# Optimization experiments

Hardware: AMD Instinct MI355X
Metric: run time of the kernel (lower is better)

The kernel has to match this reference:

```python
import jax, jax.numpy as jnp
import numpy as np

N = 32768      # total nodes
G = 64         # graphs
NPG = 512      # nodes per graph (equal-size graphs)
K = 256        # ceil(NPG * pooling_ratio), pooling_ratio=0.5
D = 256        # input_dim
H = 256        # hidden_dim
FD = 3 * H     # fusion dim
C = 10         # num_classes
E = 262144     # edges
EPS = 1e-5     # BatchNorm eps


def setup_inputs() -> dict:
    key = jax.random.key(0)
    ks = jax.random.split(key, 20)
    w = lambda k, s: jax.random.normal(k, s, jnp.float32) * 0.05
    inp = {
        'x': jax.random.normal(ks[0], (N, D), jnp.float32),
        'edge_index': jax.random.randint(ks[1], (2, E), 0, N, jnp.int64),
        'batch': (jnp.arange(N, dtype=jnp.int64) // NPG),
        'w_s1': w(ks[2], (D, H)), 'b_s1': jnp.zeros((H,), jnp.float32),
        'w_s21': w(ks[3], (D, H)), 'b_s21': jnp.zeros((H,), jnp.float32),
        'w_s22': w(ks[4], (H, H)), 'b_s22': jnp.zeros((H,), jnp.float32),
        'w_raw': w(ks[5], (D, H)), 'b_raw': jnp.zeros((H,), jnp.float32),
        'w_pos': w(ks[6], (FD, 1)), 'b_pos': jnp.zeros((1,), jnp.float32),
        'w_neg': w(ks[7], (FD, 1)), 'b_neg': jnp.zeros((1,), jnp.float32),
        'w_pool': w(ks[8], (FD, FD)), 'b_pool': jnp.zeros((FD,), jnp.float32),
        'w1': w(ks[9], (2 * FD, 256)), 'b1': jnp.zeros((256,), jnp.float32),
        'g1': jnp.ones((256,), jnp.float32), 'be1': jnp.zeros((256,), jnp.float32),
        'w2': w(ks[10], (256, 256)), 'b2': jnp.zeros((256,), jnp.float32),
        'g2': jnp.ones((256,), jnp.float32), 'be2': jnp.zeros((256,), jnp.float32),
        'w3': w(ks[11], (256, 256)), 'b3': jnp.zeros((256,), jnp.float32),
        'g3': jnp.ones((256,), jnp.float32), 'be3': jnp.zeros((256,), jnp.float32),
        'w4': w(ks[12], (256, C)), 'b4': jnp.zeros((C,), jnp.float32),
    }
    return inp


def _gcn(x, W, b, src, dst, dinv):
    # PyG GCNConv: linear, then sym-normalized aggregation with self-loops
    h = x @ W
    norm = dinv[src] * dinv[dst]
    agg = jax.ops.segment_sum(h[src] * norm[:, None], dst, num_segments=N)
    agg = agg + h * (dinv * dinv)[:, None]  # self-loop contribution
    return agg + b


def _bn(z, g, b):
    m = z.mean(0)
    v = z.var(0)  # biased, as torch BN training-mode normalization
    return (z - m) * jax.lax.rsqrt(v + EPS) * g + b


def _mlp(z, w1, b1, g1, be1, w2, b2, g2, be2, w3, b3, g3, be3, w4, b4):
    z = jax.nn.relu(_bn(z @ w1 + b1, g1, be1))  # dropout=identity (eval)
    idt = z
    o = jax.nn.relu(_bn(z @ w2 + b2, g2, be2))
    z = o + idt
    idt = z
    o = jax.nn.relu(_bn(z @ w3 + b3, g3, be3))
    z = o + idt
    return z @ w4 + b4


def _topk_mask(scores):
    # equal-size graphs -> per-graph top-k via one batched lax.top_k
    sg = scores.reshape(G, NPG)
    _, idx = jax.lax.top_k(sg, K)
    mask = jnp.zeros((G, NPG), bool).at[jnp.arange(G)[:, None], idx].set(True)
    return mask.reshape(-1)


def _readout(xt, mask):
    m = mask[:, None]
    xs = jnp.where(m, xt, 0.0).reshape(G, NPG, FD)
    mean_pool = xs.sum(1) / K
    mx = jnp.where(m, xt, -jnp.inf).reshape(G, NPG, FD).max(1)
    return jnp.concatenate([mean_pool, mx], axis=1)


def reference(x, edge_index, batch, w_s1, b_s1, w_s21, b_s21, w_s22, b_s22,
              w_raw, b_raw, w_pos, b_pos, w_neg, b_neg, w_pool, b_pool,
              w1, b1, g1, be1, w2, b2, g2, be2, w3, b3, g3, be3, w4, b4):
    src, dst = edge_index[0], edge_index[1]
    deg = jax.ops.segment_sum(jnp.ones_like(src, jnp.float32), dst, num_segments=N) + 1.0
    dinv = jax.lax.rsqrt(deg)
    lrelu = lambda z: jax.nn.leaky_relu(z, 0.01)

    h_s1 = lrelu(_gcn(x, w_s1, b_s1, src, dst, dinv))
    h_s2 = lrelu(_gcn(lrelu(_gcn(x, w_s21, b_s21, src, dst, dinv)), w_s22, b_s22, src, dst, dinv))
    h_raw = x @ w_raw + b_raw
    h_final = jnp.concatenate([h_s1, h_s2, h_raw], axis=1)  # [N, FD]

    score_pos = jax.nn.sigmoid(_gcn(h_final, w_pos, b_pos, src, dst, dinv)).reshape(-1)
    score_neg = jax.nn.sigmoid(_gcn(h_final, w_neg, b_neg, src, dst, dinv)).reshape(-1)

    xt = jax.nn.sigmoid(h_final @ w_pool + b_pool)  # pool_transform for all nodes; mask selects
    mask_pos = _topk_mask(score_pos)
    mask_neg = _topk_mask(score_neg)

    mlp = lambda e: _mlp(e, w1, b1, g1, be1, w2, b2, g2, be2, w3, b3, g3, be3, w4, b4)
    logits_pos = mlp(_readout(xt, mask_pos))
    probs_pos = jax.nn.softmax(logits_pos, axis=1)
    logits_neg = mlp(_readout(xt, mask_neg))
    probs_neg = jax.nn.softmax(logits_neg, axis=1)
    return (logits_pos, probs_pos, probs_neg, score_pos, score_neg, batch)
```

## Files before the change

### kernel.cpp

```cpp
#include <hip/hip_runtime.h>
#include <hip/hip_bf16.h>

#define N_NODES 32768
#define NGRAPH  64
#define NPG     512
#define TOPK    256
#define HID     256
#define FDIM    768
#define NEDGE   262144
#define NCLS    10
#define BN_EPS  1e-5f

#define IN_BF16 0
#define OUT_BF16 0

typedef __attribute__((ext_vector_type(8))) short short8;
typedef __attribute__((ext_vector_type(4))) float f32x4;

__device__ __forceinline__ float bf2f(unsigned short u) {
    return __uint_as_float(((unsigned)u) << 16);
}
__device__ __forceinline__ unsigned short f2bf(float f) {
    unsigned x = __float_as_uint(f);
    unsigned r = (x + 0x7fffu + ((x >> 16) & 1u)) >> 16;
    return (unsigned short)r;
}
__device__ __forceinline__ float in_ld(const void* p, size_t i) {
#if IN_BF16
    return bf2f(((const unsigned short*)p)[i]);
#else
    return ((const float*)p)[i];
#endif
}
__device__ __forceinline__ void st_out(void* o, size_t i, float v) {
#if OUT_BF16
    ((unsigned short*)o)[i] = f2bf(v);
#else
    ((float*)o)[i] = v;
#endif
}

__device__ __forceinline__ void async_cp16(const unsigned short* g, unsigned short* l) {
    __builtin_amdgcn_global_load_lds(
        (const __attribute__((address_space(1))) unsigned int*)g,
        (__attribute__((address_space(3))) unsigned int*)l, 16, 0, 0);
}

__device__ __forceinline__ void tile_swizzle(int& bm, int& bn) {
    int nx = gridDim.x;
    int L = blockIdx.y * nx + blockIdx.x;
    int xcd = L & 7;
    int j = L >> 3;
    bm = ((j / nx) * 8 + xcd) * 128;
    bn = (j % nx) * 128;
}

__global__ __launch_bounds__(256) void cvt_kernel(const float* __restrict__ in,
                                                  unsigned short* __restrict__ out, int n) {
    int i = blockIdx.x * 256 + threadIdx.x;
    if (i < n) out[i] = f2bf(in[i]);
}

__global__ __launch_bounds__(256) void cvt_t_all_kernel(const float* __restrict__ w_s1,
                                                        const float* __restrict__ w_s21,
                                                        const float* __restrict__ w_raw,
                                                        const float* __restrict__ w_s22,
                                                        const float* __restrict__ w_pool,
                                                        unsigned short* __restrict__ wcat,
                                                        unsigned short* __restrict__ wb_s22,
                                                        unsigned short* __restrict__ wb_pool) {
    __shared__ unsigned short tile[32][33];
    int id = blockIdx.x;
    const float* src;
    unsigned short* dst;
    int K, N, t;
    if (id < 64)       { src = w_s1;  dst = wcat;                       K = 256; N = 256; t = id; }
    else if (id < 128) { src = w_s21; dst = wcat + (size_t)256 * 256;   K = 256; N = 256; t = id - 64; }
    else if (id < 192) { src = w_raw; dst = wcat + (size_t)512 * 256;   K = 256; N = 256; t = id - 128; }
    else if (id < 256) { src = w_s22; dst = wb_s22;                     K = 256; N = 256; t = id - 192; }
    else               { src = w_pool; dst = wb_pool;                   K = 768; N = 768; t = id - 256; }
    int tiles_x = K >> 5;
    int bk = (t % tiles_x) * 32, bn = (t / tiles_x) * 32;
    int tx = threadIdx.x & 31, ty = threadIdx.x >> 5;
#pragma unroll
    for (int i = 0; i < 32; i += 8)
        tile[ty + i][tx] = f2bf(src[(size_t)(bk + ty + i) * N + bn + tx]);
    __syncthreads();
#pragma unroll
    for (int i = 0; i < 32; i += 8)
        dst[(size_t)(bn + ty + i) * K + bk + tx] = tile[tx][ty + i];
}

__global__ __launch_bounds__(256) void detect_kernel(const int* __restrict__ eb, int* __restrict__ flag) {
    int i = blockIdx.x * 256 + threadIdx.x;
    int v = eb[2 * (size_t)i + 1];
    unsigned long long b = __ballot(v != 0);
    if ((threadIdx.x & 63) == 0 && b)
        atomicAdd(flag, (int)__popcll(b));
}

__global__ __launch_bounds__(256) void hist_kernel(const int* __restrict__ eb, const int* __restrict__ flag,
                                                   int* __restrict__ deg) {
    int e = blockIdx.x * 256 + threadIdx.x;
    int st = (*flag == 0) ? 2 : 1;
    unsigned d = ((const unsigned*)eb)[(size_t)(NEDGE + e) * st] & (N_NODES - 1);
    atomicAdd(&deg[d], 1);
}

__global__ __launch_bounds__(1024) void scan_kernel(const int* __restrict__ cnt, int* __restrict__ rowptr,
                                                    int* __restrict__ cursor, float* __restrict__ dinv) {
    __shared__ int part[1024];
    int t = threadIdx.x;
    int base = t * 32;
    int loc[32];
    int s = 0;
#pragma unroll
    for (int i = 0; i < 32; i++) { loc[i] = cnt[base + i]; s += loc[i]; }
    part[t] = s;
    __syncthreads();
    for (int off = 1; off < 1024; off <<= 1) {
        int v = (t >= off) ? part[t - off] : 0;
        __syncthreads();
        part[t] += v;
        __syncthreads();
    }
    int run = (t == 0) ? 0 : part[t - 1];
#pragma unroll
    for (int i = 0; i < 32; i++) {
        rowptr[base + i] = run;
        cursor[base + i] = run;
        dinv[base + i] = rsqrtf((float)loc[i] + 1.0f);
        run += loc[i];
    }
    if (t == 1023) rowptr[N_NODES] = run;
}

__global__ __launch_bounds__(256) void scatter_kernel(const int* __restrict__ eb, const int* __restrict__ flag,
                                                      int* __restrict__ cursor, int* __restrict__ srcs) {
    int e = blockIdx.x * 256 + threadIdx.x;
    int st = (*flag == 0) ? 2 : 1;
    unsigned s = ((const unsigned*)eb)[(size_t)e * st] & (N_NODES - 1);
    unsigned d = ((const unsigned*)eb)[(size_t)(NEDGE + e) * st] & (N_NODES - 1);
    int p = atomicAdd(&cursor[d], 1);
    srcs[p] = (int)s;
}

#define GEMM_CORE(K_)                                                           \
    __shared__ unsigned short As[128 * 64];                                     \
    __shared__ unsigned short Bs[128 * 64];                                     \
    const int tid = threadIdx.x;                                                \
    const int wave = tid >> 6;                                                  \
    const int lane = tid & 63;                                                  \
    int bm, bn;                                                                 \
    tile_swizzle(bm, bn);                                                       \
    const int wm = (wave >> 1) * 64;                                            \
    const int wn = (wave & 1) * 64;                                             \
    const int l15 = lane & 15;                                                  \
    const int q = lane >> 4;                                                    \
    f32x4 acc[4][4] = {};                                                       \
    const int srow = lane >> 3;                                                 \
    const int schunk = lane & 7;                                                \
    const int gc = schunk ^ srow;                                               \
    const unsigned short* gaA = A + (size_t)(bm + wave * 8 + srow) * (K_) + gc * 8;  \
    const unsigned short* gbB = WT + (size_t)(bn + wave * 8 + srow) * (K_) + gc * 8; \
    const size_t K32 = (size_t)(K_) * 32;                                       \
    unsigned short* const la0 = &As[(wave * 8) * 64];                           \
    unsigned short* const lb0 = &Bs[(wave * 8) * 64];                           \
    for (int k0 = 0; k0 < (K_); k0 += 64) {                                     \
        __syncthreads();                                                        \
        _Pragma("unroll")                                                       \
        for (int t = 0; t < 4; t++) {                                           \
            async_cp16(gaA + t * K32 + k0, la0 + t * 32 * 64);                  \
            async_cp16(gbB + t * K32 + k0, lb0 + t * 32 * 64);                  \
        }                                                                       \
        __syncthreads();                                                        \
        _Pragma("unroll")                                                       \
        for (int h = 0; h < 2; h++) {                                           \
            short8 af[4], bfv[4];                                               \
            int p = (h * 4 + q) ^ (l15 & 7);                                    \
            _Pragma("unroll")                                                   \
            for (int t = 0; t < 4; t++) {                                       \
                int m = wm + t * 16 + l15;                                      \
                int n = wn + t * 16 + l15;                                      \
                af[t] = *(const short8*)&As[m * 64 + p * 8];                    \
                bfv[t] = *(const short8*)&Bs[n * 64 + p * 8];                   \
            }                                                                   \
            _Pragma("unroll")                                                   \
            for (int tm = 0; tm < 4; tm++)                                      \
                _Pragma("unroll")                                               \
                for (int tn = 0; tn < 4; tn++)                                  \
                    acc[tm][tn] = __builtin_amdgcn_mfma_f32_16x16x32_bf16(af[tm], bfv[tn], acc[tm][tn], 0, 0, 0); \
        }                                                                       \
    }

__global__ __launch_bounds__(256) void gemm_kernel(const unsigned short* __restrict__ A,
                                                   const unsigned short* __restrict__ WT,
                                                   const float* __restrict__ bias,
                                                   unsigned short* __restrict__ C,
                                                   int K, int ldC, int colOff, int epi) {
    GEMM_CORE(K)
#pragma unroll
    for (int tm = 0; tm < 4; tm++) {
        int row = bm + wm + tm * 16 + q * 4;
#pragma unroll
        for (int tn = 0; tn < 4; tn++) {
            int col = bn + wn + tn * 16 + l15;
            float bv = bias ? bias[col] : 0.0f;
#pragma unroll
            for (int r = 0; r < 4; r++) {
                float v = acc[tm][tn][r] + bv;
                if (epi == 1) v = 1.0f / (1.0f + __expf(-v));
                C[(size_t)(row + r) * ldC + colOff + col] = f2bf(v);
            }
        }
    }
}

__global__ __launch_bounds__(256) void gemm3_kernel(const unsigned short* __restrict__ A,
                                                    const unsigned short* __restrict__ WT,
                                                    const float* __restrict__ b_raw,
                                                    unsigned short* __restrict__ tA,
                                                    unsigned short* __restrict__ tB,
                                                    unsigned short* __restrict__ hfin) {
    GEMM_CORE(256)
#pragma unroll
    for (int tm = 0; tm < 4; tm++) {
        int row = bm + wm + tm * 16 + q * 4;
#pragma unroll
        for (int tn = 0; tn < 4; tn++) {
            int col = bn + wn + tn * 16 + l15;
            if (col < 256) {
#pragma unroll
                for (int r = 0; r < 4; r++)
                    tA[(size_t)(row + r) * 256 + col] = f2bf(acc[tm][tn][r]);
            } else if (col < 512) {
#pragma unroll
                for (int r = 0; r < 4; r++)
                    tB[(size_t)(row + r) * 256 + (col - 256)] = f2bf(acc[tm][tn][r]);
            } else {
                float bv = b_raw[col - 512];
#pragma unroll
                for (int r = 0; r < 4; r++)
                    hfin[(size_t)(row + r) * 768 + col] = f2bf(acc[tm][tn][r] + bv);
            }
        }
    }
}

__global__ __launch_bounds__(256) void agg2_kernel(const unsigned short* __restrict__ hA,
                                                   const unsigned short* __restrict__ hB,
                                                   const int* __restrict__ rowptr, const int* __restrict__ srcs,
                                                   const float* __restrict__ dinv,
                                                   const float* __restrict__ biasA, const float* __restrict__ biasB,
                                                   unsigned short* __restrict__ outA,
                                                   unsigned short* __restrict__ outB) {
    int wave = threadIdx.x >> 6, lane = threadIdx.x & 63;
    int v = blockIdx.x * 4 + wave;
    int f0 = lane * 4;
    float a0 = 0.f, a1 = 0.f, a2 = 0.f, a3 = 0.f;
    float c0 = 0.f, c1 = 0.f, c2 = 0.f, c3 = 0.f;
    int s = rowptr[v], e = rowptr[v + 1];
    for (int i = s; i < e; i++) {
        int u = srcs[i] & (N_NODES - 1);
        float du = dinv[u];
        uint2 ha = *(const uint2*)(hA + (size_t)u * 256 + f0);
        uint2 hb = *(const uint2*)(hB + (size_t)u * 256 + f0);
        a0 += bf2f((unsigned short)(ha.x & 0xffff)) * du;
        a1 += bf2f((unsigned short)(ha.x >> 16)) * du;
        a2 += bf2f((unsigned short)(ha.y & 0xffff)) * du;
        a3 += bf2f((unsigned short)(ha.y >> 16)) * du;
        c0 += bf2f((unsigned short)(hb.x & 0xffff)) * du;
        c1 += bf2f((unsigned short)(hb.x >> 16)) * du;
        c2 += bf2f((unsigned short)(hb.y & 0xffff)) * du;
        c3 += bf2f((unsigned short)(hb.y >> 16)) * du;
    }
    float dv = dinv[v], dv2 = dv * dv;
    uint2 sa = *(const uint2*)(hA + (size_t)v * 256 + f0);
    uint2 sb = *(const uint2*)(hB + (size_t)v * 256 + f0);
    float r0 = dv * a0 + bf2f((unsigned short)(sa.x & 0xffff)) * dv2 + biasA[f0 + 0];
    float r1 = dv * a1 + bf2f((unsigned short)(sa.x >> 16)) * dv2 + biasA[f0 + 1];
    float r2 = dv * a2 + bf2f((unsigned short)(sa.y & 0xffff)) * dv2 + biasA[f0 + 2];
    float r3 = dv * a3 + bf2f((unsigned short)(sa.y >> 16)) * dv2 + biasA[f0 + 3];
    float t0 = dv * c0 + bf2f((unsigned short)(sb.x & 0xffff)) * dv2 + biasB[f0 + 0];
    float t1 = dv * c1 + bf2f((unsigned short)(sb.x >> 16)) * dv2 + biasB[f0 + 1];
    float t2 = dv * c2 + bf2f((unsigned short)(sb.y & 0xffff)) * dv2 + biasB[f0 + 2];
    float t3 = dv * c3 + bf2f((unsigned short)(sb.y >> 16)) * dv2 + biasB[f0 + 3];
    r0 = r0 > 0.f ? r0 : 0.01f * r0;  r1 = r1 > 0.f ? r1 : 0.01f * r1;
    r2 = r2 > 0.f ? r2 : 0.01f * r2;  r3 = r3 > 0.f ? r3 : 0.01f * r3;
    t0 = t0 > 0.f ? t0 : 0.01f * t0;  t1 = t1 > 0.f ? t1 : 0.01f * t1;
    t2 = t2 > 0.f ? t2 : 0.01f * t2;  t3 = t3 > 0.f ? t3 : 0.01f * t3;
    uint2 ov = make_uint2(((unsigned)f2bf(r1) << 16) | f2bf(r0), ((unsigned)f2bf(r3) << 16) | f2bf(r2));
    uint2 ow = make_uint2(((unsigned)f2bf(t1) << 16) | f2bf(t0), ((unsigned)f2bf(t3) << 16) | f2bf(t2));
    *(uint2*)(outA + (size_t)v * 768 + f0) = ov;
    *(uint2*)(outB + (size_t)v * 256 + f0) = ow;
}

__global__ __launch_bounds__(256) void agg_kernel(const unsigned short* __restrict__ h,
                                                  const int* __restrict__ rowptr, const int* __restrict__ srcs,
                                                  const float* __restrict__ dinv, const float* __restrict__ bias,
                                                  unsigned short* __restrict__ out, int ldOut, int colOff,
                                                  int do_lrelu) {
    int wave = threadIdx.x >> 6, lane = threadIdx.x & 63;
    int v = blockIdx.x * 4 + wave;
    int f0 = lane * 4;
    float a0 = 0.f, a1 = 0.f, a2 = 0.f, a3 = 0.f;
    int s = rowptr[v], e = rowptr[v + 1];
    for (int i = s; i < e; i++) {
        int u = srcs[i] & (N_NODES - 1);
        float du = dinv[u];
        uint2 hv = *(const uint2*)(h + (size_t)u * 256 + f0);
        a0 += bf2f((unsigned short)(hv.x & 0xffff)) * du;
        a1 += bf2f((unsigned short)(hv.x >> 16)) * du;
        a2 += bf2f((unsigned short)(hv.y & 0xffff)) * du;
        a3 += bf2f((unsigned short)(hv.y >> 16)) * du;
    }
    float dv = dinv[v], dv2 = dv * dv;
    uint2 sv = *(const uint2*)(h + (size_t)v * 256 + f0);
    float r0 = dv * a0 + bf2f((unsigned short)(sv.x & 0xffff)) * dv2 + bias[f0 + 0];
    float r1 = dv * a1 + bf2f((unsigned short)(sv.x >> 16)) * dv2 + bias[f0 + 1];
    float r2 = dv * a2 + bf2f((unsigned short)(sv.y & 0xffff)) * dv2 + bias[f0 + 2];
    float r3 = dv * a3 + bf2f((unsigned short)(sv.y >> 16)) * dv2 + bias[f0 + 3];
    if (do_lrelu) {
        r0 = r0 > 0.f ? r0 : 0.01f * r0;
        r1 = r1 > 0.f ? r1 : 0.01f * r1;
        r2 = r2 > 0.f ? r2 : 0.01f * r2;
        r3 = r3 > 0.f ? r3 : 0.01f * r3;
    }
    uint2 ov = make_uint2(((unsigned)f2bf(r1) << 16) | f2bf(r0), ((unsigned)f2bf(r3) << 16) | f2bf(r2));
    *(uint2*)(out + (size_t)v * ldOut + colOff + f0) = ov;
}

__global__ __launch_bounds__(256) void score_mv_kernel(const unsigned short* __restrict__ hf,
                                                       const void* __restrict__ wp, const void* __restrict__ wn,
                                                       float* __restrict__ svp, float* __restrict__ svn) {
    int wave = threadIdx.x >> 6, lane = threadIdx.x & 63;
    int v = blockIdx.x * 4 + wave;
    float sp = 0.f, sn = 0.f;
#pragma unroll
    for (int i = 0; i < 3; i++) {
        int k = i * 256 + lane * 4;
        uint2 hv = *(const uint2*)(hf + (size_t)v * 768 + k);
        float x0 = bf2f((unsigned short)(hv.x & 0xffff));
        float x1 = bf2f((unsigned short)(hv.x >> 16));
        float x2 = bf2f((unsigned short)(hv.y & 0xffff));
        float x3 = bf2f((unsigned short)(hv.y >> 16));
        sp += x0 * in_ld(wp, k) + x1 * in_ld(wp, k + 1) + x2 * in_ld(wp, k + 2) + x3 * in_ld(wp, k + 3);
        sn += x0 * in_ld(wn, k) + x1 * in_ld(wn, k + 1) + x2 * in_ld(wn, k + 2) + x3 * in_ld(wn, k + 3);
    }
    for (int off = 32; off >= 1; off >>= 1) {
        sp += __shfl_down(sp, off, 64);
        sn += __shfl_down(sn, off, 64);
    }
    if (lane == 0) { svp[v] = sp; svn[v] = sn; }
}

__global__ __launch_bounds__(256) void score_agg_kernel(const float* __restrict__ svp, const float* __restrict__ svn,
                                                        const int* __restrict__ rowptr, const int* __restrict__ srcs,
                                                        const float* __restrict__ dinv,
                                                        const void* __restrict__ bp, const void* __restrict__ bn_,
                                                        float* __restrict__ scp, float* __restrict__ scn,
                                                        void* __restrict__ dout) {
    int v = blockIdx.x * 256 + threadIdx.x;
    float ap = 0.f, an = 0.f;
    int s = rowptr[v], e = rowptr[v + 1];
    for (int i = s; i < e; i++) {
        int u = srcs[i] & (N_NODES - 1);
        float du = dinv[u];
        ap += svp[u] * du;
        an += svn[u] * du;
    }
    float dv = dinv[v], dv2 = dv * dv;
    float zp = dv * ap + svp[v] * dv2 + in_ld(bp, 0);
    float zn = dv * an + svn[v] * dv2 + in_ld(bn_, 0);
    float pp = 1.0f / (1.0f + __expf(-zp));
    float pn = 1.0f / (1.0f + __expf(-zn));
    scp[v] = pp;
    scn[v] = pn;
    st_out(dout, 1920 + (size_t)v, pp);
    st_out(dout, 1920 + (size_t)N_NODES + v, pn);
    st_out(dout, 1920 + 2 * (size_t)N_NODES + v, (float)(v >> 9));
}

__global__ __launch_bounds__(512) void topk2_kernel(const float* __restrict__ scp, const float* __restrict__ scn,
                                                    unsigned char* __restrict__ maskp,
                                                    unsigned char* __restrict__ maskn) {
    __shared__ float s[512];
    const float* sc = (blockIdx.x & 1) ? scn : scp;
    unsigned char* mask = (blockIdx.x & 1) ? maskn : maskp;
    int g = blockIdx.x >> 1, i = threadIdx.x;
    float my = sc[(size_t)g * 512 + i];
    s[i] = my;
    __syncthreads();
    int cnt = 0;
    for (int j = 0; j < 512; j++) {
        float o = s[j];
        cnt += (int)((o > my) || ((o == my) && (j < i)));
    }
    mask[(size_t)g * 512 + i] = (cnt < TOPK) ? 1 : 0;
}

__global__ __launch_bounds__(256) void readout2_kernel(const unsigned short* __restrict__ xt,
                                                       const unsigned char* __restrict__ maskp,
                                                       const unsigned char* __restrict__ maskn,
                                                       float* __restrict__ eout) {
    int g = blockIdx.x;
    int c = blockIdx.y;
    int wv = threadIdx.x >> 6, lane = threadIdx.x & 63;
    int f = c * 64 + lane;
    __shared__ unsigned char mp[512], mn[512];
    __shared__ float red[4][64][4];
    for (int i = threadIdx.x; i < 512; i += 256) {
        mp[i] = maskp[(size_t)g * 512 + i];
        mn[i] = maskn[(size_t)g * 512 + i];
    }
    __syncthreads();
    float sp = 0.f, sn = 0.f, xp = -INFINITY, xn = -INFINITY;
    const unsigned short* base = xt + ((size_t)g * 512 + wv * 128) * 768 + f;
    for (int v = 0; v < 128; v++) {
        unsigned char bp = mp[wv * 128 + v], bn_ = mn[wv * 128 + v];
        if (!(bp | bn_)) continue;
        float x = bf2f(base[(size_t)v * 768]);
        if (bp) { sp += x; xp = fmaxf(xp, x); }
        if (bn_) { sn += x; xn = fmaxf(xn, x); }
    }
    red[wv][lane][0] = sp; red[wv][lane][1] = xp;
    red[wv][lane][2] = sn; red[wv][lane][3] = xn;
    __syncthreads();
    if (wv == 0) {
#pragma unroll
        for (int w = 1; w < 4; w++) {
            sp += red[w][lane][0]; xp = fmaxf(xp, red[w][lane][1]);
            sn += red[w][lane][2]; xn = fmaxf(xn, red[w][lane][3]);
        }
        float* erp = eout + (size_t)g * 1536;
        float* ern = eout + (size_t)(64 + g) * 1536;
        erp[f] = sp * (1.0f / TOPK);
        erp[768 + f] = xp;
        ern[f] = sn * (1.0f / TOPK);
        ern[768 + f] = xn;
    }
}

__global__ __launch_bounds__(256) void mlp_gemm2_kernel(const float* __restrict__ in,
                                                        const float* __restrict__ W,
                                                        const float* __restrict__ b,
                                                        float* __restrict__ out, int K) {
    __shared__ float row[1536];
    __shared__ float red[4][64];
    int r = blockIdx.x, cg = blockIdx.y;
    int wv = threadIdx.x >> 6, lane = threadIdx.x & 63;
    int c = cg * 64 + lane;
    for (int k = threadIdx.x; k < K; k += 256) row[k] = in[(size_t)r * K + k];
    __syncthreads();
    int kpw = K >> 2;
    const float* wp = W + (size_t)(wv * kpw) * 256 + c;
    const float* rp = row + wv * kpw;
    float acc = 0.f;
#pragma unroll 4
    for (int k = 0; k < kpw; k++)
        acc += rp[k] * wp[(size_t)k * 256];
    red[wv][lane] = acc;
    __syncthreads();
    if (wv == 0) {
        float v = red[0][lane] + red[1][lane] + red[2][lane] + red[3][lane] + b[c];
        out[(size_t)r * 256 + c] = v;
    }
}

__global__ __launch_bounds__(64) void bn_kernel(const float* __restrict__ z, const void* __restrict__ gamma,
                                                const void* __restrict__ beta, const float* __restrict__ res,
                                                float* __restrict__ out) {
    int f = blockIdx.x & 255, g = blockIdx.x >> 8, r = threadIdx.x;
    size_t idx = (size_t)(g * 64 + r) * 256 + f;
    float x = z[idx];
    float s = x, sq = x * x;
    for (int off = 1; off < 64; off <<= 1) {
        s += __shfl_xor(s, off, 64);
        sq += __shfl_xor(sq, off, 64);
    }
    float m = s * (1.0f / 64.0f);
    float var = sq * (1.0f / 64.0f) - m * m;
    float y = (x - m) * rsqrtf(var + BN_EPS) * in_ld(gamma, f) + in_ld(beta, f);
    y = fmaxf(y, 0.0f);
    if (res) y += res[idx];
    out[idx] = y;
}

__global__ __launch_bounds__(64) void logits_kernel(const float* __restrict__ act, const void* __restrict__ w4,
                                                    const void* __restrict__ b4, float* __restrict__ lg) {
    int idx = blockIdx.x * 64 + threadIdx.x;
    if (idx >= 128 * NCLS) return;
    int r = idx / NCLS, c = idx % NCLS;
    float acc = in_ld(b4, c);
    for (int k = 0; k < 256; k++) acc += act[(size_t)r * 256 + k] * in_ld(w4, (size_t)k * NCLS + c);
    lg[idx] = acc;
}

__global__ __launch_bounds__(64) void softmax_kernel(const float* __restrict__ lg, void* __restrict__ dout) {
    int r = blockIdx.x * 64 + threadIdx.x;
    if (r >= 128) return;
    float l[NCLS];
    float mx = -1e30f;
    for (int c = 0; c < NCLS; c++) { l[c] = lg[(size_t)r * NCLS + c]; mx = fmaxf(mx, l[c]); }
    float sum = 0.f;
    float ex[NCLS];
    for (int c = 0; c < NCLS; c++) { ex[c] = __expf(l[c] - mx); sum += ex[c]; }
    float inv = 1.0f / sum;
    int g = r >> 6, rr = r & 63;
    if (g == 0) {
        for (int c = 0; c < NCLS; c++) st_out(dout, (size_t)rr * NCLS + c, l[c]);
        for (int c = 0; c < NCLS; c++) st_out(dout, 640 + (size_t)rr * NCLS + c, ex[c] * inv);
    } else {
        for (int c = 0; c < NCLS; c++) st_out(dout, 1280 + (size_t)rr * NCLS + c, ex[c] * inv);
    }
}

extern "C" void kernel_launch(void* const* d_in, const int* in_sizes, int n_in,
                              void* d_out, int out_size, void* d_ws, size_t ws_size,
                              hipStream_t stream) {
    (void)in_sizes; (void)n_in; (void)out_size; (void)ws_size;

    const float* x = (const float*)d_in[0];
    const int* eb = (const int*)d_in[1];
    const float* w_s1 = (const float*)d_in[3];
    const float* b_s1 = (const float*)d_in[4];
    const float* w_s21 = (const float*)d_in[5];
    const float* b_s21 = (const float*)d_in[6];
    const float* w_s22 = (const float*)d_in[7];
    const float* b_s22 = (const float*)d_in[8];
    const float* w_raw = (const float*)d_in[9];
    const float* b_raw = (const float*)d_in[10];
    const void* w_pos = d_in[11];
    const void* b_pos = d_in[12];
    const void* w_neg = d_in[13];
    const void* b_neg = d_in[14];
    const float* w_pool = (const float*)d_in[15];
    const float* b_pool = (const float*)d_in[16];
    const float* w1 = (const float*)d_in[17];  const float* b1 = (const float*)d_in[18];
    const void* g1 = d_in[19];  const void* be1 = d_in[20];
    const float* w2 = (const float*)d_in[21];  const float* b2 = (const float*)d_in[22];
    const void* g2 = d_in[23];  const void* be2 = d_in[24];
    const float* w3 = (const float*)d_in[25];  const float* b3 = (const float*)d_in[26];
    const void* g3 = d_in[27];  const void* be3 = d_in[28];
    const void* w4 = d_in[29];  const void* b4 = d_in[30];

    char* ws = (char*)d_ws;
    size_t off = 0;
    auto alloc = [&](size_t b) -> void* {
        void* p = ws + off;
        off += (b + 255) & ~(size_t)255;
        return p;
    };
    int* flag = (int*)alloc(256);
    int* deg = (int*)alloc((size_t)N_NODES * 4);
    float* dinv = (float*)alloc((size_t)N_NODES * 4);
    int* rowptr = (int*)alloc((size_t)(N_NODES + 1) * 4);
    int* cursor = (int*)alloc((size_t)N_NODES * 4);
    int* srcs = (int*)alloc((size_t)NEDGE * 4);
    unsigned short* xbf = (unsigned short*)alloc((size_t)N_NODES * 256 * 2);
    unsigned short* wcat = (unsigned short*)alloc((size_t)768 * 256 * 2);
    unsigned short* wb_s22 = (unsigned short*)alloc((size_t)256 * 256 * 2);
    unsigned short* wb_pool = (unsigned short*)alloc((size_t)768 * 768 * 2);
    unsigned short* tA = (unsigned short*)alloc((size_t)N_NODES * 256 * 2);
    unsigned short* tB = (unsigned short*)alloc((size_t)N_NODES * 256 * 2);
    unsigned short* tmpB = (unsigned short*)alloc((size_t)N_NODES * 256 * 2);
    unsigned short* hfin = (unsigned short*)alloc((size_t)N_NODES * 768 * 2);
    unsigned short* xt = (unsigned short*)alloc((size_t)N_NODES * 768 * 2);
    float* svp = (float*)alloc((size_t)N_NODES * 4);
    float* svn = (float*)alloc((size_t)N_NODES * 4);
    float* scp = (float*)alloc((size_t)N_NODES * 4);
    float* scn = (float*)alloc((size_t)N_NODES * 4);
    unsigned char* maskp = (unsigned char*)alloc(N_NODES);
    unsigned char* maskn = (unsigned char*)alloc(N_NODES);
    float* ebuf = (float*)alloc((size_t)128 * 1536 * 4);
    float* zb = (float*)alloc((size_t)128 * 256 * 4);
    float* act1 = (float*)alloc((size_t)128 * 256 * 4);
    float* act2 = (float*)alloc((size_t)128 * 256 * 4);
    float* act3 = (float*)alloc((size_t)128 * 256 * 4);
    float* lg = (float*)alloc((size_t)128 * NCLS * 4);

    hipMemsetAsync(flag, 0, 256, stream);
    hipMemsetAsync(deg, 0, (size_t)N_NODES * 4, stream);
    detect_kernel<<<NEDGE / 256, 256, 0, stream>>>(eb, flag);
    hist_kernel<<<NEDGE / 256, 256, 0, stream>>>(eb, flag, deg);
    scan_kernel<<<1, 1024, 0, stream>>>(deg, rowptr, cursor, dinv);
    scatter_kernel<<<NEDGE / 256, 256, 0, stream>>>(eb, flag, cursor, srcs);

    cvt_kernel<<<(N_NODES * 256 + 255) / 256, 256, 0, stream>>>(x, xbf, N_NODES * 256);
    cvt_t_all_kernel<<<832, 256, 0, stream>>>(w_s1, w_s21, w_raw, w_s22, w_pool, wcat, wb_s22, wb_pool);

    dim3 gG3(768 / 128, N_NODES / 128);
    dim3 gA(256 / 128, N_NODES / 128);
    dim3 gP(768 / 128, N_NODES / 128);

    gemm3_kernel<<<gG3, 256, 0, stream>>>(xbf, wcat, b_raw, tA, tB, hfin);
    agg2_kernel<<<N_NODES / 4, 256, 0, stream>>>(tA, tB, rowptr, srcs, dinv, b_s1, b_s21, hfin, tmpB);
    gemm_kernel<<<gA, 256, 0, stream>>>(tmpB, wb_s22, nullptr, tA, 256, 256, 0, 0);
    agg_kernel<<<N_NODES / 4, 256, 0, stream>>>(tA, rowptr, srcs, dinv, b_s22, hfin, 768, 256, 1);
    gemm_kernel<<<gP, 256, 0, stream>>>(hfin, wb_pool, b_pool, xt, 768, 768, 0, 1);
    score_mv_kernel<<<N_NODES / 4, 256, 0, stream>>>(hfin, w_pos, w_neg, svp, svn);
    score_agg_kernel<<<N_NODES / 256, 256, 0, stream>>>(svp, svn, rowptr, srcs, dinv, b_pos, b_neg, scp, scn, d_out);
    topk2_kernel<<<2 * NGRAPH, 512, 0, stream>>>(scp, scn, maskp, maskn);
    {
        dim3 gR(NGRAPH, FDIM / 64);
        readout2_kernel<<<gR, 256, 0, stream>>>(xt, maskp, maskn, ebuf);
    }
    {
        dim3 gM(128, 4);
        mlp_gemm2_kernel<<<gM, 256, 0, stream>>>(ebuf, w1, b1, zb, 1536);
        bn_kernel<<<512, 64, 0, stream>>>(zb, g1, be1, nullptr, act1);
        mlp_gemm2_kernel<<<gM, 256, 0, stream>>>(act1, w2, b2, zb, 256);
        bn_kernel<<<512, 64, 0, stream>>>(zb, g2, be2, act1, act2);
        mlp_gemm2_kernel<<<gM, 256, 0, stream>>>(act2, w3, b3, zb, 256);
        bn_kernel<<<512, 64, 0, stream>>>(zb, g3, be3, act2, act3);
    }
    logits_kernel<<<(128 * NCLS + 63) / 64, 64, 0, stream>>>(act3, w4, b4, lg);
    softmax_kernel<<<2, 64, 0, stream>>>(lg, d_out);
}
```

Measured before the change: 601.8 us.

## Aggregate before linear in GCN layers and fold score projections into pool GEMM

Reorders each GCN as (Â·X)·W instead of Â·(X·W). The first aggregation now runs once on the 256-wide input and feeds a 512-wide GEMM that applies bias and leaky ReLU in its epilogue, replacing the dual-buffer aggregation. The score matrix-vector products are folded into the pool GEMM by appending w_pos/w_neg as extra weight rows padded to 896. The x conversion and weight transposes are merged into one vectorized launch. This trades the separate score kernel and intermediate buffers for roughly 17% wasted GEMM columns, an extra GEMM launch for the raw branch, and a slightly different bf16 rounding order.

```diff
diff --git a/kernel.cpp b/kernel.cpp
--- a/kernel.cpp
+++ b/kernel.cpp
@@ -55,30 +55,46 @@
     bn = (j % nx) * 128;
 }
 
-__global__ __launch_bounds__(256) void cvt_kernel(const float* __restrict__ in,
-                                                  unsigned short* __restrict__ out, int n) {
-    int i = blockIdx.x * 256 + threadIdx.x;
-    if (i < n) out[i] = f2bf(in[i]);
-}
-
-__global__ __launch_bounds__(256) void cvt_t_all_kernel(const float* __restrict__ w_s1,
-                                                        const float* __restrict__ w_s21,
-                                                        const float* __restrict__ w_raw,
-                                                        const float* __restrict__ w_s22,
-                                                        const float* __restrict__ w_pool,
-                                                        unsigned short* __restrict__ wcat,
-                                                        unsigned short* __restrict__ wb_s22,
-                                                        unsigned short* __restrict__ wb_pool) {
+__global__ __launch_bounds__(256) void cvt_all_kernel(const float* __restrict__ x,
+                                                      const float* __restrict__ w_s1,
+                                                      const float* __restrict__ w_s21,
+                                                      const float* __restrict__ w_s22,
+                                                      const float* __restrict__ w_raw,
+                                                      const float* __restrict__ w_pool,
+                                                      const float* __restrict__ w_pos,
+                                                      const float* __restrict__ w_neg,
+                                                      unsigned short* __restrict__ xbf,
+                                                      unsigned short* __restrict__ wcat2,
+                                                      unsigned short* __restrict__ wb_s22,
+                                                      unsigned short* __restrict__ wb_raw,
+                                                      unsigned short* __restrict__ wpool896) {
+    int id = blockIdx.x;
+    if (id < 4096) {
+        size_t base = (size_t)id * 2048 + threadIdx.x * 8;
+        float4 a = *(const float4*)(x + base);
+        float4 b = *(const float4*)(x + base + 4);
+        unsigned short o[8] = { f2bf(a.x), f2bf(a.y), f2bf(a.z), f2bf(a.w),
+                                f2bf(b.x), f2bf(b.y), f2bf(b.z), f2bf(b.w) };
+        *(uint4*)(xbf + base) = *(uint4*)o;
+        return;
+    }
+    if (id >= 4928) {
+        int j = id - 4928;
+        const float* src = (j < 3) ? w_pos : w_neg;
+        int seg = (j < 3) ? j : j - 3;
+        size_t row = (j < 3) ? 768 : 769;
+        wpool896[row * 768 + seg * 256 + threadIdx.x] = f2bf(src[seg * 256 + threadIdx.x]);
+        return;
+    }
     __shared__ unsigned short tile[32][33];
-    int id = blockIdx.x;
     const float* src;
     unsigned short* dst;
     int K, N, t;
-    if (id < 64)       { src = w_s1;  dst = wcat;                       K = 256; N = 256; t = id; }
-    else if (id < 128) { src = w_s21; dst = wcat + (size_t)256 * 256;   K = 256; N = 256; t = id - 64; }
-    else if (id < 192) { src = w_raw; dst = wcat + (size_t)512 * 256;   K = 256; N = 256; t = id - 128; }
-    else if (id < 256) { src = w_s22; dst = wb_s22;                     K = 256; N = 256; t = id - 192; }
-    else               { src = w_pool; dst = wb_pool;                   K = 768; N = 768; t = id - 256; }
+    if (id < 4160)      { src = w_s1;  dst = wcat2;                     K = 256; N = 256; t = id - 4096; }
+    else if (id < 4224) { src = w_s21; dst = wcat2 + (size_t)256 * 256; K = 256; N = 256; t = id - 4160; }
+    else if (id < 4288) { src = w_s22; dst = wb_s22;                    K = 256; N = 256; t = id - 4224; }
+    else if (id < 4352) { src = w_raw; dst = wb_raw;                    K = 256; N = 256; t = id - 4288; }
+    else                { src = w_pool; dst = wpool896;                 K = 768; N = 768; t = id - 4352; }
     int tiles_x = K >> 5;
     int bk = (t % tiles_x) * 32, bn = (t / tiles_x) * 32;
     int tx = threadIdx.x & 31, ty = threadIdx.x >> 5;
@@ -210,18 +226,19 @@
             for (int r = 0; r < 4; r++) {
                 float v = acc[tm][tn][r] + bv;
                 if (epi == 1) v = 1.0f / (1.0f + __expf(-v));
+                else if (epi == 2) v = v > 0.f ? v : 0.01f * v;
                 C[(size_t)(row + r) * ldC + colOff + col] = f2bf(v);
             }
         }
     }
 }
 
-__global__ __launch_bounds__(256) void gemm3_kernel(const unsigned short* __restrict__ A,
+__global__ __launch_bounds__(256) void gemmA_kernel(const unsigned short* __restrict__ A,
                                                     const unsigned short* __restrict__ WT,
-                                                    const float* __restrict__ b_raw,
-                                                    unsigned short* __restrict__ tA,
-                                                    unsigned short* __restrict__ tB,
-                                                    unsigned short* __restrict__ hfin) {
+                                                    const float* __restrict__ b_s1,
+                                                    const float* __restrict__ b_s21,
+                                                    unsigned short* __restrict__ hfin,
+                                                    unsigned short* __restrict__ t1) {
     GEMM_CORE(256)
 #pragma unroll
     for (int tm = 0; tm < 4; tm++) {
@@ -230,76 +247,62 @@
         for (int tn = 0; tn < 4; tn++) {
             int col = bn + wn + tn * 16 + l15;
             if (col < 256) {
-#pragma unroll
-                for (int r = 0; r < 4; r++)
-                    tA[(size_t)(row + r) * 256 + col] = f2bf(acc[tm][tn][r]);
-            } else if (col < 512) {
-#pragma unroll
-                for (int r = 0; r < 4; r++)
-                    tB[(size_t)(row + r) * 256 + (col - 256)] = f2bf(acc[tm][tn][r]);
+                float bv = b_s1[col];
+#pragma unroll
+                for (int r = 0; r < 4; r++) {
+                    float v = acc[tm][tn][r] + bv;
+                    v = v > 0.f ? v : 0.01f * v;
+                    hfin[(size_t)(row + r) * 768 + col] = f2bf(v);
+                }
             } else {
-                float bv = b_raw[col - 512];
-#pragma unroll
-                for (int r = 0; r < 4; r++)
-                    hfin[(size_t)(row + r) * 768 + col] = f2bf(acc[tm][tn][r] + bv);
+                float bv = b_s21[col - 256];
+#pragma unroll
+                for (int r = 0; r < 4; r++) {
+                    float v = acc[tm][tn][r] + bv;
+                    v = v > 0.f ? v : 0.01f * v;
+                    t1[(size_t)(row + r) * 256 + (col - 256)] = f2bf(v);
+                }
             }
         }
     }
 }
 
-__global__ __launch_bounds__(256) void agg2_kernel(const unsigned short* __restrict__ hA,
-                                                   const unsigned short* __restrict__ hB,
-                                                   const int* __restrict__ rowptr, const int* __restrict__ srcs,
-                                                   const float* __restrict__ dinv,
-                                                   const float* __restrict__ biasA, const float* __restrict__ biasB,
-                                                   unsigned short* __restrict__ outA,
-                                                   unsigned short* __restrict__ outB) {
-    int wave = threadIdx.x >> 6, lane = threadIdx.x & 63;
-    int v = blockIdx.x * 4 + wave;
-    int f0 = lane * 4;
-    float a0 = 0.f, a1 = 0.f, a2 = 0.f, a3 = 0.f;
-    float c0 = 0.f, c1 = 0.f, c2 = 0.f, c3 = 0.f;
-    int s = rowptr[v], e = rowptr[v + 1];
-    for (int i = s; i < e; i++) {
-        int u = srcs[i] & (N_NODES - 1);
-        float du = dinv[u];
-        uint2 ha = *(const uint2*)(hA + (size_t)u * 256 + f0);
-        uint2 hb = *(const uint2*)(hB + (size_t)u * 256 + f0);
-        a0 += bf2f((unsigned short)(ha.x & 0xffff)) * du;
-        a1 += bf2f((unsigned short)(ha.x >> 16)) * du;
-        a2 += bf2f((unsigned short)(ha.y & 0xffff)) * du;
-        a3 += bf2f((unsigned short)(ha.y >> 16)) * du;
-        c0 += bf2f((unsigned short)(hb.x & 0xffff)) * du;
-        c1 += bf2f((unsigned short)(hb.x >> 16)) * du;
-        c2 += bf2f((unsigned short)(hb.y & 0xffff)) * du;
-        c3 += bf2f((unsigned short)(hb.y >> 16)) * du;
-    }
-    float dv = dinv[v], dv2 = dv * dv;
-    uint2 sa = *(const uint2*)(hA + (size_t)v * 256 + f0);
-    uint2 sb = *(const uint2*)(hB + (size_t)v * 256 + f0);
-    float r0 = dv * a0 + bf2f((unsigned short)(sa.x & 0xffff)) * dv2 + biasA[f0 + 0];
-    float r1 = dv * a1 + bf2f((unsigned short)(sa.x >> 16)) * dv2 + biasA[f0 + 1];
-    float r2 = dv * a2 + bf2f((unsigned short)(sa.y & 0xffff)) * dv2 + biasA[f0 + 2];
-    float r3 = dv * a3 + bf2f((unsigned short)(sa.y >> 16)) * dv2 + biasA[f0 + 3];
-    float t0 = dv * c0 + bf2f((unsigned short)(sb.x & 0xffff)) * dv2 + biasB[f0 + 0];
-    float t1 = dv * c1 + bf2f((unsigned short)(sb.x >> 16)) * dv2 + biasB[f0 + 1];
-    float t2 = dv * c2 + bf2f((unsigned short)(sb.y & 0xffff)) * dv2 + biasB[f0 + 2];
-    float t3 = dv * c3 + bf2f((unsigned short)(sb.y >> 16)) * dv2 + biasB[f0 + 3];
-    r0 = r0 > 0.f ? r0 : 0.01f * r0;  r1 = r1 > 0.f ? r1 : 0.01f * r1;
-    r2 = r2 > 0.f ? r2 : 0.01f * r2;  r3 = r3 > 0.f ? r3 : 0.01f * r3;
-    t0 = t0 > 0.f ? t0 : 0.01f * t0;  t1 = t1 > 0.f ? t1 : 0.01f * t1;
-    t2 = t2 > 0.f ? t2 : 0.01f * t2;  t3 = t3 > 0.f ? t3 : 0.01f * t3;
-    uint2 ov = make_uint2(((unsigned)f2bf(r1) << 16) | f2bf(r0), ((unsigned)f2bf(r3) << 16) | f2bf(r2));
-    uint2 ow = make_uint2(((unsigned)f2bf(t1) << 16) | f2bf(t0), ((unsigned)f2bf(t3) << 16) | f2bf(t2));
-    *(uint2*)(outA + (size_t)v * 768 + f0) = ov;
-    *(uint2*)(outB + (size_t)v * 256 + f0) = ow;
-}
-
-__global__ __launch_bounds__(256) void agg_kernel(const unsigned short* __restrict__ h,
-                                                  const int* __restrict__ rowptr, const int* __restrict__ srcs,
-                                                  const float* __restrict__ dinv, const float* __restrict__ bias,
-                                                  unsigned short* __restrict__ out, int ldOut, int colOff,
-                                                  int do_lrelu) {
+__global__ __launch_bounds__(256) void gemmP_kernel(const unsigned short* __restrict__ A,
+                                                    const unsigned short* __restrict__ WT,
+                                                    const float* __restrict__ b_pool,
+                                                    unsigned short* __restrict__ xt,
+                                                    float* __restrict__ svp, float* __restrict__ svn,
+                                                    int K) {
+    GEMM_CORE(K)
+#pragma unroll
+    for (int tm = 0; tm < 4; tm++) {
+        int row = bm + wm + tm * 16 + q * 4;
+#pragma unroll
+        for (int tn = 0; tn < 4; tn++) {
+            int col = bn + wn + tn * 16 + l15;
+            if (col < 768) {
+                float bv = b_pool[col];
+#pragma unroll
+                for (int r = 0; r < 4; r++) {
+                    float v = acc[tm][tn][r] + bv;
+                    v = 1.0f / (1.0f + __expf(-v));
+                    xt[(size_t)(row + r) * 768 + col] = f2bf(v);
+                }
+            } else if (col == 768) {
+#pragma unroll
+                for (int r = 0; r < 4; r++) svp[row + r] = acc[tm][tn][r];
+            } else if (col == 769) {
+#pragma unroll
+                for (int r = 0; r < 4; r++) svn[row + r] = acc[tm][tn][r];
+            }
+        }
+    }
+}
+
+__global__ __launch_bounds__(256) void lin_agg_kernel(const unsigned short* __restrict__ h,
+                                                      const int* __restrict__ rowptr, const int* __restrict__ srcs,
+                                                      const float* __restrict__ dinv,
+                                                      unsigned short* __restrict__ out) {
     int wave = threadIdx.x >> 6, lane = threadIdx.x & 63;
     int v = blockIdx.x * 4 + wave;
     int f0 = lane * 4;
@@ -316,42 +319,12 @@
     }
     float dv = dinv[v], dv2 = dv * dv;
     uint2 sv = *(const uint2*)(h + (size_t)v * 256 + f0);
-    float r0 = dv * a0 + bf2f((unsigned short)(sv.x & 0xffff)) * dv2 + bias[f0 + 0];
-    float r1 = dv * a1 + bf2f((unsigned short)(sv.x >> 16)) * dv2 + bias[f0 + 1];
-    float r2 = dv * a2 + bf2f((unsigned short)(sv.y & 0xffff)) * dv2 + bias[f0 + 2];
-    float r3 = dv * a3 + bf2f((unsigned short)(sv.y >> 16)) * dv2 + bias[f0 + 3];
-    if (do_lrelu) {
-        r0 = r0 > 0.f ? r0 : 0.01f * r0;
-        r1 = r1 > 0.f ? r1 : 0.01f * r1;
-        r2 = r2 > 0.f ? r2 : 0.01f * r2;
-        r3 = r3 > 0.f ? r3 : 0.01f * r3;
-    }
+    float r0 = dv * a0 + bf2f((unsigned short)(sv.x & 0xffff)) * dv2;
+    float r1 = dv * a1 + bf2f((unsigned short)(sv.x >> 16)) * dv2;
+    float r2 = dv * a2 + bf2f((unsigned short)(sv.y & 0xffff)) * dv2;
+    float r3 = dv * a3 + bf2f((unsigned short)(sv.y >> 16)) * dv2;
     uint2 ov = make_uint2(((unsigned)f2bf(r1) << 16) | f2bf(r0), ((unsigned)f2bf(r3) << 16) | f2bf(r2));
-    *(uint2*)(out + (size_t)v * ldOut + colOff + f0) = ov;
-}
-
-__global__ __launch_bounds__(256) void score_mv_kernel(const unsigned short* __restrict__ hf,
-                                                       const void* __restrict__ wp, const void* __restrict__ wn,
-                                                       float* __restrict__ svp, float* __restrict__ svn) {
-    int wave = threadIdx.x >> 6, lane = threadIdx.x & 63;
-    int v = blockIdx.x * 4 + wave;
-    float sp = 0.f, sn = 0.f;
-#pragma unroll
-    for (int i = 0; i < 3; i++) {
-        int k = i * 256 + lane * 4;
-        uint2 hv = *(const uint2*)(hf + (size_t)v * 768 + k);
-        float x0 = bf2f((unsigned short)(hv.x & 0xffff));
-        float x1 = bf2f((unsigned short)(hv.x >> 16));
-        float x2 = bf2f((unsigned short)(hv.y & 0xffff));
-        float x3 = bf2f((unsigned short)(hv.y >> 16));
-        sp += x0 * in_ld(wp, k) + x1 * in_ld(wp, k + 1) + x2 * in_ld(wp, k + 2) + x3 * in_ld(wp, k + 3);
-        sn += x0 * in_ld(wn, k) + x1 * in_ld(wn, k + 1) + x2 * in_ld(wn, k + 2) + x3 * in_ld(wn, k + 3);
-    }
-    for (int off = 32; off >= 1; off >>= 1) {
-        sp += __shfl_down(sp, off, 64);
-        sn += __shfl_down(sn, off, 64);
-    }
-    if (lane == 0) { svp[v] = sp; svn[v] = sn; }
+    *(uint2*)(out + (size_t)v * 256 + f0) = ov;
 }
 
 __global__ __launch_bounds__(256) void score_agg_kernel(const float* __restrict__ svp, const float* __restrict__ svn,
@@ -530,9 +503,9 @@
     const float* b_s22 = (const float*)d_in[8];
     const float* w_raw = (const float*)d_in[9];
     const float* b_raw = (const float*)d_in[10];
-    const void* w_pos = d_in[11];
+    const float* w_pos = (const float*)d_in[11];
     const void* b_pos = d_in[12];
-    const void* w_neg = d_in[13];
+    const float* w_neg = (const float*)d_in[13];
     const void* b_neg = d_in[14];
     const float* w_pool = (const float*)d_in[15];
     const float* b_pool = (const float*)d_in[16];
@@ -558,12 +531,13 @@
     int* cursor = (int*)alloc((size_t)N_NODES * 4);
     int* srcs = (int*)alloc((size_t)NEDGE * 4);
     unsigned short* xbf = (unsigned short*)alloc((size_t)N_NODES * 256 * 2);
-    unsigned short* wcat = (unsigned short*)alloc((size_t)768 * 256 * 2);
+    unsigned short* wcat2 = (unsigned short*)alloc((size_t)512 * 256 * 2);
     unsigned short* wb_s22 = (unsigned short*)alloc((size_t)256 * 256 * 2);
-    unsigned short* wb_pool = (unsigned short*)alloc((size_t)768 * 768 * 2);
-    unsigned short* tA = (unsigned short*)alloc((size_t)N_NODES * 256 * 2);
-    unsigned short* tB = (unsigned short*)alloc((size_t)N_NODES * 256 * 2);
-    unsigned short* tmpB = (unsigned short*)alloc((size_t)N_NODES * 256 * 2);
+    unsigned short* wb_raw = (unsigned short*)alloc((size_t)256 * 256 * 2);
+    unsigned short* wpool896 = (unsigned short*)alloc((size_t)896 * 768 * 2);
+    unsigned short* Xa = (unsigned short*)alloc((size_t)N_NODES * 256 * 2);
+    unsigned short* t1 = (unsigned short*)alloc((size_t)N_NODES * 256 * 2);
+    unsigned short* t1a = (unsigned short*)alloc((size_t)N_NODES * 256 * 2);
     unsigned short* hfin = (unsigned short*)alloc((size_t)N_NODES * 768 * 2);
     unsigned short* xt = (unsigned short*)alloc((size_t)N_NODES * 768 * 2);
     float* svp = (float*)alloc((size_t)N_NODES * 4);
@@ -581,24 +555,26 @@
 
     hipMemsetAsync(flag, 0, 256, stream);
     hipMemsetAsync(deg, 0, (size_t)N_NODES * 4, stream);
+    hipMemsetAsync(wpool896 + (size_t)770 * 768, 0, (size_t)126 * 768 * 2, stream);
+
     detect_kernel<<<NEDGE / 256, 256, 0, stream>>>(eb, flag);
     hist_kernel<<<NEDGE / 256, 256, 0, stream>>>(eb, flag, deg);
     scan_kernel<<<1, 1024, 0, stream>>>(deg, rowptr, cursor, dinv);
     scatter_kernel<<<NEDGE / 256, 256, 0, stream>>>(eb, flag, cursor, srcs);
 
-    cvt_kernel<<<(N_NODES * 256 + 255) / 256, 256, 0, stream>>>(x, xbf, N_NODES * 256);
-    cvt_t_all_kernel<<<832, 256, 0, stream>>>(w_s1, w_s21, w_raw, w_s22, w_pool, wcat, wb_s22, wb_pool);
-
-    dim3 gG3(768 / 128, N_NODES / 128);
-    dim3 gA(256 / 128, N_NODES / 128);
-    dim3 gP(768 / 128, N_NODES / 128);
-
-    gemm3_kernel<<<gG3, 256, 0, stream>>>(xbf, wcat, b_raw, tA, tB, hfin);
-    agg2_kernel<<<N_NODES / 4, 256, 0, stream>>>(tA, tB, rowptr, srcs, dinv, b_s1, b_s21, hfin, tmpB);
-    gemm_kernel<<<gA, 256, 0, stream>>>(tmpB, wb_s22, nullptr, tA, 256, 256, 0, 0);
-    agg_kernel<<<N_NODES / 4, 256, 0, stream>>>(tA, rowptr, srcs, dinv, b_s22, hfin, 768, 256, 1);
-    gemm_kernel<<<gP, 256, 0, stream>>>(hfin, wb_pool, b_pool, xt, 768, 768, 0, 1);
-    score_mv_kernel<<<N_NODES / 4, 256, 0, stream>>>(hfin, w_pos, w_neg, svp, svn);
+    cvt_all_kernel<<<4934, 256, 0, stream>>>(x, w_s1, w_s21, w_s22, w_raw, w_pool, w_pos, w_neg,
+                                             xbf, wcat2, wb_s22, wb_raw, wpool896);
+
+    dim3 gA2(512 / 128, N_NODES / 128);
+    dim3 gA1(256 / 128, N_NODES / 128);
+    dim3 gP(896 / 128, N_NODES / 128);
+
+    lin_agg_kernel<<<N_NODES / 4, 256, 0, stream>>>(xbf, rowptr, srcs, dinv, Xa);
+    gemmA_kernel<<<gA2, 256, 0, stream>>>(Xa, wcat2, b_s1, b_s21, hfin, t1);
+    lin_agg_kernel<<<N_NODES / 4, 256, 0, stream>>>(t1, rowptr, srcs, dinv, t1a);
+    gemm_kernel<<<gA1, 256, 0, stream>>>(t1a, wb_s22, b_s22, hfin, 256, 768, 256, 2);
+    gemm_kernel<<<gA1, 256, 0, stream>>>(xbf, wb_raw, b_raw, hfin, 256, 768, 512, 0);
+    gemmP_kernel<<<gP, 256, 0, stream>>>(hfin, wpool896, b_pool, xt, svp, svn, 768);
     score_agg_kernel<<<N_NODES / 256, 256, 0, stream>>>(svp, svn, rowptr, srcs, dinv, b_pos, b_neg, scp, scn, d_out);
     topk2_kernel<<<2 * NGRAPH, 512, 0, stream>>>(scp, scn, maskp, maskn);
     {
```

Measured after the change: 589.6 us. 1.02x faster.
